# Performance work log

Hardware: AMD Instinct MI355X
Metric: run time of the kernel (lower is better)

Reference implementation:

```python
import jax, jax.numpy as jnp
import numpy as np

N = 1024      # number of stocks
D_FEAT = 6    # features per day
T = 60        # lookback window
HID = 64      # GRU hidden size
R = 60        # number of relation types


def setup_inputs() -> dict:
    key = jax.random.key(0)
    ks = jax.random.split(key, 10)
    s = 1.0 / np.sqrt(HID)
    u = lambda k, shape: jax.random.uniform(k, shape, jnp.float32, -s, s)
    inp = {
        "x": jax.random.normal(ks[0], (N, D_FEAT * T), jnp.float32),
        "relation_matrix": (jax.random.uniform(ks[1], (N, N, R)) < 0.02).astype(jnp.float32),
        # GRU params (PyTorch layout: W_ih [3H, D], W_hh [3H, H])
        "W_ih": u(ks[2], (3 * HID, D_FEAT)),
        "W_hh": u(ks[3], (3 * HID, HID)),
        "b_ih": u(ks[4], (3 * HID,)),
        "b_hh": u(ks[5], (3 * HID,)),
        # attention linear W: Linear(2H+R, 1) -> weight vector + bias
        "w_att": jax.random.normal(ks[6], (2 * HID + R,), jnp.float32) * 0.05,
        "b_att": u(ks[7], (1,)),
        "W_fc": u(ks[8], (1, 2 * HID)),
        "b_fc": u(ks[9], (1,)),
    }
    return inp


def reference(x, relation_matrix, W_ih, W_hh, b_ih, b_hh, w_att, b_att, W_fc, b_fc):
    n = x.shape[0]
    H = W_hh.shape[1]
    # [N, D*T] -> [N, D, T] -> [N, T, D] -> [T, N, D] for scan over time
    xh = x.reshape(n, D_FEAT, -1).transpose(0, 2, 1)
    xs = jnp.transpose(xh, (1, 0, 2))

    def gru_step(h, xt):
        gi = xt @ W_ih.T + b_ih          # [N, 3H]
        gh = h @ W_hh.T + b_hh           # [N, 3H]
        i_r, i_z, i_n = jnp.split(gi, 3, axis=1)
        h_r, h_z, h_n = jnp.split(gh, 3, axis=1)
        r = jax.nn.sigmoid(i_r + h_r)
        z = jax.nn.sigmoid(i_z + h_z)
        nn_ = jnp.tanh(i_n + r * h_n)
        return (1.0 - z) * nn_ + z * h, None

    h0 = jnp.zeros((n, H), x.dtype)
    h_last, _ = jax.lax.scan(gru_step, h0, xs)  # [N, H] (last timestep)

    # concat-attention score: W([e_i || e_j || rel_ij]) decomposed to avoid
    # materializing the [N, N, 2H+R] concat tensor (same math as torch)
    w_ei, w_ej, w_rel = w_att[:H], w_att[H:2 * H], w_att[2 * H:]
    s_i = h_last @ w_ei                                   # [N]
    s_j = h_last @ w_ej                                   # [N]
    s_rel = jnp.einsum('ijr,r->ij', relation_matrix, w_rel)  # [N, N]
    weight = s_i[:, None] + s_j[None, :] + s_rel + b_att[0]
    weight = jnp.where(weight >= 0, weight, 0.01 * weight)   # LeakyReLU(0.01)

    mask = (jnp.sum(relation_matrix, axis=2) != 0).astype(x.dtype)  # [N, N]
    temp = mask * weight
    temp = jnp.where(temp == 0, jnp.asarray(-10000.0, x.dtype), temp)
    valid = jax.nn.softmax(temp, axis=1) * mask

    agg = valid @ h_last                                  # [N, H]
    hidden = jnp.concatenate([h_last, agg], axis=1)       # [N, 2H]
    out = (hidden @ W_fc.T + b_fc)[:, 0]                  # [N]
    return out
```

## Files before the change

### kernel.cpp

```cpp
#include <hip/hip_runtime.h>

#define NN 1024
#define DFEAT 6
#define TSTEPS 60
#define HID 64
#define RREL 60
#define SENT -1.0e30f

__global__ __launch_bounds__(256) void fused_kernel(
    const float* __restrict__ x,
    const float* __restrict__ W_ih,
    const float* __restrict__ W_hh,
    const float* __restrict__ b_ih,
    const float* __restrict__ b_hh,
    const float* __restrict__ w_att,
    const float* __restrict__ rel,
    float* __restrict__ h_last,
    float* __restrict__ s_i,
    float* __restrict__ s_j,
    float* __restrict__ temp)
{
    if (blockIdx.x >= NN) {
        const int b = blockIdx.x - NN;
        const int i = b >> 2;
        const int j = ((b & 3) << 8) + threadIdx.x;
        const size_t pair = (size_t)i * NN + j;

        float wrel[RREL];
#pragma unroll
        for (int r = 0; r < RREL; ++r) wrel[r] = w_att[2 * HID + r];

        const float4* rp = reinterpret_cast<const float4*>(rel + pair * RREL);
        float srel = 0.0f, msum = 0.0f;
#pragma unroll
        for (int r4 = 0; r4 < RREL / 4; ++r4) {
            float4 v = rp[r4];
            srel += v.x * wrel[4*r4+0] + v.y * wrel[4*r4+1]
                  + v.z * wrel[4*r4+2] + v.w * wrel[4*r4+3];
            msum += v.x + v.y + v.z + v.w;
        }
        temp[pair] = (msum != 0.0f) ? srel : SENT;
        return;
    }

    const int n = blockIdx.x;
    const int g = threadIdx.x;

    __shared__ __align__(16) float x_sh[DFEAT * TSTEPS];
    __shared__ __align__(16) float h_sh[HID];
    __shared__ float gi_sh[192];
    __shared__ float gh_sh[192];

    for (int idx = g; idx < DFEAT * TSTEPS; idx += 256)
        x_sh[idx] = x[(size_t)n * (DFEAT * TSTEPS) + idx];

    float whh[HID];
    float wih[DFEAT];
    float bih = 0.0f, bhh = 0.0f;
    if (g < 192) {
#pragma unroll
        for (int k4 = 0; k4 < HID / 4; ++k4) {
            float4 w = *reinterpret_cast<const float4*>(&W_hh[g * HID + k4 * 4]);
            whh[k4 * 4 + 0] = w.x; whh[k4 * 4 + 1] = w.y;
            whh[k4 * 4 + 2] = w.z; whh[k4 * 4 + 3] = w.w;
        }
#pragma unroll
        for (int d = 0; d < DFEAT; ++d) wih[d] = W_ih[g * DFEAT + d];
        bih = b_ih[g];
        bhh = b_hh[g];
    }

    if (g < HID) h_sh[g] = 0.0f;
    __syncthreads();

    for (int t = 0; t < TSTEPS; ++t) {
        if (g < 192) {
            float gi = bih;
#pragma unroll
            for (int d = 0; d < DFEAT; ++d) gi += x_sh[d * TSTEPS + t] * wih[d];

            float gh = bhh;
#pragma unroll
            for (int k4 = 0; k4 < HID / 4; ++k4) {
                float4 hv = *reinterpret_cast<const float4*>(&h_sh[k4 * 4]);
                gh += hv.x * whh[k4 * 4 + 0] + hv.y * whh[k4 * 4 + 1]
                    + hv.z * whh[k4 * 4 + 2] + hv.w * whh[k4 * 4 + 3];
            }
            gi_sh[g] = gi;
            gh_sh[g] = gh;
        }
        __syncthreads();

        if (g < HID) {
            float ir = gi_sh[g],        hr = gh_sh[g];
            float iz = gi_sh[HID + g],  hz = gh_sh[HID + g];
            float in_ = gi_sh[2*HID + g], hn = gh_sh[2*HID + g];
            float r = 1.0f / (1.0f + __expf(-(ir + hr)));
            float z = 1.0f / (1.0f + __expf(-(iz + hz)));
            float nn_ = tanhf(in_ + r * hn);
            float hold = h_sh[g];
            h_sh[g] = (1.0f - z) * nn_ + z * hold;
        }
        __syncthreads();
    }

    if (g < HID) {
        float hv = h_sh[g];
        h_last[(size_t)n * HID + g] = hv;
        float pi = hv * w_att[g];
        float pj = hv * w_att[HID + g];
#pragma unroll
        for (int off = 32; off > 0; off >>= 1) {
            pi += __shfl_down(pi, off);
            pj += __shfl_down(pj, off);
        }
        if (g == 0) { s_i[n] = pi; s_j[n] = pj; }
    }
}

__global__ __launch_bounds__(256) void row_kernel(
    const float* __restrict__ temp,
    const float* __restrict__ s_i,
    const float* __restrict__ s_j,
    const float* __restrict__ b_att,
    const float* __restrict__ h_last,
    const float* __restrict__ W_fc,
    const float* __restrict__ b_fc,
    float* __restrict__ out)
{
    const int i = blockIdx.x;
    const int tid = threadIdx.x;

    __shared__ __align__(16) float pm_sh[NN];
    __shared__ float red_sh[256];

    const float si_b = s_i[i] + b_att[0];
    float4 sv = reinterpret_cast<const float4*>(temp + (size_t)i * NN)[tid];
    float4 sj = reinterpret_cast<const float4*>(s_j)[tid];

    float tvv[4];
    {
        float srels[4] = {sv.x, sv.y, sv.z, sv.w};
        float sjs[4]   = {sj.x, sj.y, sj.z, sj.w};
#pragma unroll
        for (int c = 0; c < 4; ++c) {
            float w = si_b + sjs[c] + srels[c];
            w = (w >= 0.0f) ? w : 0.01f * w;
            float tv = (srels[c] != SENT) ? w : 0.0f;
            tvv[c] = (tv == 0.0f) ? -10000.0f : tv;
        }
    }
    float m = fmaxf(fmaxf(tvv[0], tvv[1]), fmaxf(tvv[2], tvv[3]));
    red_sh[tid] = m;
    __syncthreads();
    for (int s = 128; s > 0; s >>= 1) {
        if (tid < s) red_sh[tid] = fmaxf(red_sh[tid], red_sh[tid + s]);
        __syncthreads();
    }
    const float M = red_sh[0];
    __syncthreads();

    float lsum = 0.0f;
    float4 pmv;
    {
        float e0 = __expf(tvv[0] - M), e1 = __expf(tvv[1] - M);
        float e2 = __expf(tvv[2] - M), e3 = __expf(tvv[3] - M);
        lsum = e0 + e1 + e2 + e3;
        pmv.x = (tvv[0] != -10000.0f) ? e0 : 0.0f;
        pmv.y = (tvv[1] != -10000.0f) ? e1 : 0.0f;
        pmv.z = (tvv[2] != -10000.0f) ? e2 : 0.0f;
        pmv.w = (tvv[3] != -10000.0f) ? e3 : 0.0f;
    }
    reinterpret_cast<float4*>(pm_sh)[tid] = pmv;

    red_sh[tid] = lsum;
    __syncthreads();
    for (int s = 128; s > 0; s >>= 1) {
        if (tid < s) red_sh[tid] += red_sh[tid + s];
        __syncthreads();
    }
    const float invS = 1.0f / red_sh[0];
    __syncthreads();

    const int h = tid & (HID - 1);
    const int grp = tid >> 6;
    float part = 0.0f;
    const float* hl = h_last + (size_t)grp * 256 * HID + h;
    const float* pm = pm_sh + grp * 256;
    for (int jc = 0; jc < 256; ++jc)
        part += pm[jc] * hl[(size_t)jc * HID];

    red_sh[tid] = part;
    __syncthreads();

    if (tid < HID) {
        float agg = (red_sh[tid] + red_sh[HID + tid]
                   + red_sh[2 * HID + tid] + red_sh[3 * HID + tid]) * invS;
        float o = h_last[(size_t)i * HID + tid] * W_fc[tid] + agg * W_fc[HID + tid];
#pragma unroll
        for (int off = 32; off > 0; off >>= 1) o += __shfl_down(o, off);
        if (tid == 0) out[i] = o + b_fc[0];
    }
}

extern "C" void kernel_launch(void* const* d_in, const int* in_sizes, int n_in,
                              void* d_out, int out_size, void* d_ws, size_t ws_size,
                              hipStream_t stream) {
    const float* x     = (const float*)d_in[0];
    const float* rel   = (const float*)d_in[1];
    const float* W_ih  = (const float*)d_in[2];
    const float* W_hh  = (const float*)d_in[3];
    const float* b_ih  = (const float*)d_in[4];
    const float* b_hh  = (const float*)d_in[5];
    const float* w_att = (const float*)d_in[6];
    const float* b_att = (const float*)d_in[7];
    const float* W_fc  = (const float*)d_in[8];
    const float* b_fc  = (const float*)d_in[9];

    float* ws     = (float*)d_ws;
    float* h_last = ws;
    float* s_i    = ws + NN * HID;
    float* s_j    = ws + NN * HID + NN;
    float* temp   = ws + NN * HID + 2 * NN;

    fused_kernel<<<NN + NN * 4, 256, 0, stream>>>(
        x, W_ih, W_hh, b_ih, b_hh, w_att, rel, h_last, s_i, s_j, temp);
    row_kernel<<<NN, 256, 0, stream>>>(temp, s_i, s_j, b_att, h_last,
                                       W_fc, b_fc, (float*)d_out);
}
```

Baseline: 97.81 us.

## Coalesce relation-tensor reads with 16-lane rows and DPP reductions

The relation reduction blocks now handle one full row i each. Sixteen lanes cooperatively read one pair's 60 relation values as float4 chunks, so global loads are contiguous across the wavefront instead of each thread striding 240 bytes. Partial dot products and mask sums are combined with DPP row reductions, and the grid shrinks from 4096 to 1024 relation blocks. The cost is extra cross-lane reduction instructions, one idle lane per 16, and fewer but longer-running blocks.

Result: slower. 102.4 us (+4.7%).

```diff
diff --git a/kernel.cpp b/kernel.cpp
--- a/kernel.cpp
+++ b/kernel.cpp
@@ -6,6 +6,19 @@
 #define HID 64
 #define RREL 60
 #define SENT -1.0e30f
+
+__device__ __forceinline__ float row16_reduce_add(float x) {
+    int t;
+    t = __builtin_amdgcn_update_dpp(0, __float_as_int(x), 0x128, 0xf, 0xf, false);
+    x += __int_as_float(t);
+    t = __builtin_amdgcn_update_dpp(0, __float_as_int(x), 0x124, 0xf, 0xf, false);
+    x += __int_as_float(t);
+    t = __builtin_amdgcn_update_dpp(0, __float_as_int(x), 0x122, 0xf, 0xf, false);
+    x += __int_as_float(t);
+    t = __builtin_amdgcn_update_dpp(0, __float_as_int(x), 0x121, 0xf, 0xf, false);
+    x += __int_as_float(t);
+    return x;
+}
 
 __global__ __launch_bounds__(256) void fused_kernel(
     const float* __restrict__ x,
@@ -21,25 +34,38 @@
     float* __restrict__ temp)
 {
     if (blockIdx.x >= NN) {
-        const int b = blockIdx.x - NN;
-        const int i = b >> 2;
-        const int j = ((b & 3) << 8) + threadIdx.x;
-        const size_t pair = (size_t)i * NN + j;
-
-        float wrel[RREL];
-#pragma unroll
-        for (int r = 0; r < RREL; ++r) wrel[r] = w_att[2 * HID + r];
-
-        const float4* rp = reinterpret_cast<const float4*>(rel + pair * RREL);
-        float srel = 0.0f, msum = 0.0f;
-#pragma unroll
-        for (int r4 = 0; r4 < RREL / 4; ++r4) {
-            float4 v = rp[r4];
-            srel += v.x * wrel[4*r4+0] + v.y * wrel[4*r4+1]
-                  + v.z * wrel[4*r4+2] + v.w * wrel[4*r4+3];
-            msum += v.x + v.y + v.z + v.w;
-        }
-        temp[pair] = (msum != 0.0f) ? srel : SENT;
+        const int i    = blockIdx.x - NN;
+        const int lane = threadIdx.x & 63;
+        const int wv   = threadIdx.x >> 6;
+        const int rr   = lane >> 4;
+        const int chunk = lane & 15;
+        const int cc   = (chunk < 15) ? chunk : 14;
+        const bool c15 = (chunk == 15);
+
+        float4 wr = *reinterpret_cast<const float4*>(&w_att[2 * HID + cc * 4]);
+        if (c15) { wr.x = 0.0f; wr.y = 0.0f; wr.z = 0.0f; wr.w = 0.0f; }
+
+        const float* rowbase = rel + (size_t)i * (NN * RREL);
+
+        for (int it = 0; it < 16; ++it) {
+            const int jb = wv * 256 + it * 16 + rr;
+            float4 v[4];
+#pragma unroll
+            for (int u = 0; u < 4; ++u) {
+                const float* p = rowbase + (size_t)(jb + u * 4) * RREL + cc * 4;
+                v[u] = *reinterpret_cast<const float4*>(p);
+            }
+#pragma unroll
+            for (int u = 0; u < 4; ++u) {
+                float pd = v[u].x * wr.x + v[u].y * wr.y
+                         + v[u].z * wr.z + v[u].w * wr.w;
+                float pm = c15 ? 0.0f : (v[u].x + v[u].y + v[u].z + v[u].w);
+                pd = row16_reduce_add(pd);
+                pm = row16_reduce_add(pm);
+                if (chunk == 0)
+                    temp[(size_t)i * NN + jb + u * 4] = (pm != 0.0f) ? pd : SENT;
+            }
+        }
         return;
     }
 
@@ -223,7 +249,7 @@
     float* s_j    = ws + NN * HID + NN;
     float* temp   = ws + NN * HID + 2 * NN;
 
-    fused_kernel<<<NN + NN * 4, 256, 0, stream>>>(
+    fused_kernel<<<NN + NN, 256, 0, stream>>>(
         x, W_ih, W_hh, b_ih, b_hh, w_att, rel, h_last, s_i, s_j, temp);
     row_kernel<<<NN, 256, 0, stream>>>(temp, s_i, s_j, b_att, h_last,
                                        W_fc, b_fc, (float*)d_out);
```
